# Optimization experiments

Hardware: AMD Instinct MI355X
Metric: run time of the kernel (lower is better)

The kernel has to match this reference:

```python
import jax, jax.numpy as jnp
import numpy as np

EMBED = 1024
HEADS = 16
HEAD_DIM = EMBED // HEADS


def setup_inputs() -> dict:
    key = jax.random.key(0)
    ks = jax.random.split(key, 8)
    N, L = 2, 2048
    s = 0.02
    return {
        "values": jax.random.normal(ks[0], (N, L, EMBED), jnp.float32),
        "keys": jax.random.normal(ks[1], (N, L, EMBED), jnp.float32),
        "queries": jax.random.normal(ks[2], (N, L, EMBED), jnp.float32),
        # per-head projection weights, SHARED across heads (nn.Linear(head_dim, head_dim))
        "Wv": jax.random.normal(ks[3], (HEAD_DIM, HEAD_DIM), jnp.float32) * s,
        "Wk": jax.random.normal(ks[4], (HEAD_DIM, HEAD_DIM), jnp.float32) * s,
        "Wq": jax.random.normal(ks[5], (HEAD_DIM, HEAD_DIM), jnp.float32) * s,
        "Wo": jax.random.normal(ks[6], (EMBED, EMBED), jnp.float32) * s,
        "bo": jax.random.normal(ks[7], (EMBED,), jnp.float32) * s,
    }


def reference(values, keys, queries, Wv, Wk, Wq, Wo, bo):
    N, Lq, _ = queries.shape
    Lk = keys.shape[1]
    Lv = values.shape[1]
    # split heads: (N, L, H, D)
    v = values.reshape(N, Lv, HEADS, HEAD_DIM)
    k = keys.reshape(N, Lk, HEADS, HEAD_DIM)
    q = queries.reshape(N, Lq, HEADS, HEAD_DIM)
    # per-head linear (weight shared across heads); nn.Linear computes x @ W.T
    v = jnp.einsum('nlhd,ed->nlhe', v, Wv)
    k = jnp.einsum('nlhd,ed->nlhe', k, Wk)
    q = jnp.einsum('nlhd,ed->nlhe', q, Wq)
    # scores (N, H, Lq, Lk); NOTE: scale uses sqrt(embed_size), as in the original
    scores = jnp.einsum('nqhd,nkhd->nhqk', q, k) / jnp.sqrt(jnp.float32(EMBED))
    attn = jax.nn.softmax(scores, axis=-1)
    out = jnp.einsum('nhql,nlhd->nqhd', attn, v).reshape(N, Lq, EMBED)
    out = out @ Wo.T + bo
    return out
```

## Files before the change

kernel.cpp:

```cpp
#include <hip/hip_runtime.h>
#include <hip/hip_bf16.h>

#define EMBED 1024
#define HEADS 16
#define HD 64
#define NB 2
#define LSEQ 2048

typedef __bf16 bf16x8 __attribute__((ext_vector_type(8)));
typedef float f32x4 __attribute__((ext_vector_type(4)));

static __device__ __forceinline__ __bf16 f2b(float x) {
    union { __hip_bfloat16 h; __bf16 b; } u;
    u.h = __float2bfloat16(x);
    return u.b;
}
static __device__ __forceinline__ bf16x8 cvt8(float4 a, float4 b) {
    bf16x8 r;
    r[0] = f2b(a.x); r[1] = f2b(a.y); r[2] = f2b(a.z); r[3] = f2b(a.w);
    r[4] = f2b(b.x); r[5] = f2b(b.y); r[6] = f2b(b.z); r[7] = f2b(b.w);
    return r;
}
static __device__ __forceinline__ unsigned short b2u(float x) {
    union { __hip_bfloat16 h; unsigned short u; } c;
    c.h = __float2bfloat16(x);
    return c.u;
}

#define GLD16(g, l) __builtin_amdgcn_global_load_lds( \
    (const __attribute__((address_space(1))) void*)(g), \
    (__attribute__((address_space(3))) void*)(l), 16, 0, 0)


__global__ __launch_bounds__(256) void proj_kernel(
    const float* __restrict__ vals,
    const float* __restrict__ keys,
    const float* __restrict__ quer,
    const float* __restrict__ Wv,
    const float* __restrict__ Wk,
    const float* __restrict__ Wq,
    __hip_bfloat16* __restrict__ QF,
    __hip_bfloat16* __restrict__ KF,
    __hip_bfloat16* __restrict__ VF)
{
    int b      = blockIdx.x;
    int tensor = b % 3;
    int rem    = b / 3;
    int n      = rem >> 7;
    int lt     = (rem >> 2) & 31;
    int hg     = rem & 3;
    int t = threadIdx.x, w = t >> 6, lane = t & 63;
    int m16 = lane & 15, quad = lane >> 4;
    int l0 = lt * 64 + w * 16;

    const float* X = (tensor == 0) ? quer : (tensor == 1 ? keys : vals);
    const float* W = (tensor == 0) ? Wq   : (tensor == 1 ? Wk   : Wv);
    float scale = (tensor == 0) ? (1.44269504088896340736f / 32.0f) : 1.0f;

    bf16x8 wf[4][2];
#pragma unroll
    for (int f = 0; f < 4; ++f)
#pragma unroll
        for (int kk = 0; kk < 2; ++kk) {
            const float* wp = W + (f * 16 + m16) * HD + kk * 32 + quad * 8;
            wf[f][kk] = cvt8(*(const float4*)wp, *(const float4*)(wp + 4));
        }

#pragma unroll
    for (int hh = 0; hh < 4; ++hh) {
        int h = hg * 4 + hh;
        const float* xb = X + ((size_t)n * LSEQ + l0 + m16) * EMBED + h * HD + quad * 8;
        bf16x8 xf[2];
#pragma unroll
        for (int kk = 0; kk < 2; ++kk)
            xf[kk] = cvt8(*(const float4*)(xb + kk * 32), *(const float4*)(xb + kk * 32 + 4));

        size_t nhb = (size_t)(n * HEADS + h) * 131072;
        if (tensor != 2) {
            f32x4 acc[4] = {};
#pragma unroll
            for (int f = 0; f < 4; ++f) {
                acc[f] = __builtin_amdgcn_mfma_f32_16x16x32_bf16(wf[f][0], xf[0], acc[f], 0, 0, 0);
                acc[f] = __builtin_amdgcn_mfma_f32_16x16x32_bf16(wf[f][1], xf[1], acc[f], 0, 0, 0);
            }
            int key = l0 + m16;
#pragma unroll
            for (int f = 0; f < 4; ++f) {
                union { ushort4 u; unsigned short s[4]; } p;
#pragma unroll
                for (int r = 0; r < 4; ++r) p.s[r] = b2u(acc[f][r] * scale);
                int kk   = f >> 1;
                int qk2  = (f & 1) * 2 + (quad >> 1);
                int j4   = (quad & 1) * 4;
                __hip_bfloat16* dst;
                if (tensor == 0) {
                    dst = QF + nhb + (size_t)(l0 >> 4) * 1024 + kk * 512
                        + (qk2 * 16 + m16) * 8 + j4;
                } else {
                    dst = KF + nhb + (size_t)(key >> 5) * 2048
                        + ((key & 1) * 2 + kk) * 512
                        + (qk2 * 16 + ((key & 31) >> 1)) * 8 + j4;
                }
                *(ushort4*)dst = p.u;
            }
        } else {
            f32x4 acc[4] = {};
#pragma unroll
            for (int f = 0; f < 4; ++f) {
                acc[f] = __builtin_amdgcn_mfma_f32_16x16x32_bf16(xf[0], wf[f][0], acc[f], 0, 0, 0);
                acc[f] = __builtin_amdgcn_mfma_f32_16x16x32_bf16(xf[1], wf[f][1], acc[f], 0, 0, 0);
            }
            int keyq  = l0 + quad * 4;
            int c     = keyq >> 5;
            int quadv = (keyq & 31) >> 3;
            int j4    = (quad & 1) * 4;
#pragma unroll
            for (int f = 0; f < 4; ++f) {
                union { ushort4 u; unsigned short s[4]; } p;
#pragma unroll
                for (int r = 0; r < 4; ++r) p.s[r] = b2u(acc[f][r]);
                __hip_bfloat16* dst = VF + nhb + (size_t)c * 2048 + f * 512
                    + quadv * 128 + m16 * 8 + j4;
                *(ushort4*)dst = p.u;
            }
        }
    }
}

__global__ __launch_bounds__(256) void wcvt_kernel(
    const float* __restrict__ Wo, __hip_bfloat16* __restrict__ Wob)
{
    int base = (blockIdx.x * 256 + threadIdx.x) * 16;
#pragma unroll
    for (int j = 0; j < 16; j += 4) {
        float4 w4 = *(const float4*)(Wo + base + j);
        __hip_bfloat16 o[4] = {
            __float2bfloat16(w4.x), __float2bfloat16(w4.y),
            __float2bfloat16(w4.z), __float2bfloat16(w4.w)};
        *(ushort4*)(Wob + base + j) = *(const ushort4*)o;
    }
}

#define CHUNKS 32
__global__ __launch_bounds__(256) void attn_kernel(
    const __hip_bfloat16* __restrict__ QF,
    const __hip_bfloat16* __restrict__ KF,
    const __hip_bfloat16* __restrict__ VF,
    __hip_bfloat16* __restrict__ AO)
{
    __shared__ __align__(16) __hip_bfloat16 Pb[2][4][32][40];

    int i  = blockIdx.x;
    int x  = i & 7, r2 = i >> 3;
    int nh = x * 4 + (r2 >> 5);
    int qblk = r2 & 31;

    int t = threadIdx.x, w = t >> 6, lane = t & 63;
    int m16 = lane & 15, quad = lane >> 4;
    int qh = w & 1, kh = w >> 1;
    int q0 = qblk * 64 + qh * 32;
    size_t nhb = (size_t)nh * 131072;

    const __hip_bfloat16* qb = QF + nhb + (size_t)(q0 >> 4) * 1024 + lane * 8;
    bf16x8 qf[2][2];
#pragma unroll
    for (int tq = 0; tq < 2; ++tq)
#pragma unroll
        for (int kk = 0; kk < 2; ++kk)
            qf[tq][kk] = *(const bf16x8*)(qb + tq * 1024 + kk * 512);

    const __hip_bfloat16* kp = KF + nhb + (size_t)(kh * 32) * 2048 + lane * 8;
    const __hip_bfloat16* vp = VF + nhb + (size_t)(kh * 32) * 2048 + lane * 8;

    f32x4 of[2][4] = {};
    float ls[2][4] = {};
    bf16x8 kf[2][2], vf[4], pf[2];

#pragma unroll 1
    for (int c = 0; c <= CHUNKS; ++c) {
        if (c < CHUNKS) {
            const __hip_bfloat16* kc = kp + (size_t)c * 2048;
            kf[0][0] = *(const bf16x8*)(kc);
            kf[0][1] = *(const bf16x8*)(kc + 512);
            kf[1][0] = *(const bf16x8*)(kc + 1024);
            kf[1][1] = *(const bf16x8*)(kc + 1536);
        }
        if (c > 0) {
            pf[0] = *(const bf16x8*)&Pb[(c - 1) & 1][w][m16][quad * 8];
            pf[1] = *(const bf16x8*)&Pb[(c - 1) & 1][w][16 + m16][quad * 8];
#pragma unroll
            for (int tq = 0; tq < 2; ++tq)
#pragma unroll
                for (int f = 0; f < 4; ++f)
                    of[tq][f] = __builtin_amdgcn_mfma_f32_16x16x32_bf16(
                        pf[tq], vf[f], of[tq][f], 0, 0, 0);
        }
        if (c < CHUNKS) {
            const __hip_bfloat16* vc = vp + (size_t)c * 2048;
#pragma unroll
            for (int f = 0; f < 4; ++f)
                vf[f] = *(const bf16x8*)(vc + f * 512);

            f32x4 s[2][2];
#pragma unroll
            for (int tq = 0; tq < 2; ++tq)
#pragma unroll
                for (int t2 = 0; t2 < 2; ++t2) {
                    f32x4 z = {};
                    z = __builtin_amdgcn_mfma_f32_16x16x32_bf16(qf[tq][0], kf[t2][0], z, 0, 0, 0);
                    z = __builtin_amdgcn_mfma_f32_16x16x32_bf16(qf[tq][1], kf[t2][1], z, 0, 0, 0);
                    s[tq][t2] = z;
                }
#pragma unroll
            for (int tq = 0; tq < 2; ++tq)
#pragma unroll
                for (int r = 0; r < 4; ++r) {
                    float e0 = __builtin_amdgcn_exp2f(s[tq][0][r]);
                    float e1 = __builtin_amdgcn_exp2f(s[tq][1][r]);
                    ls[tq][r] += e0 + e1;
                    unsigned u = __builtin_amdgcn_perm(
                        __float_as_uint(e1), __float_as_uint(e0), 0x07060302);
                    *(unsigned*)&Pb[c & 1][w][tq * 16 + quad * 4 + r][2 * m16] = u;
                }
        }
    }

#pragma unroll
    for (int tq = 0; tq < 2; ++tq)
#pragma unroll
        for (int r = 0; r < 4; ++r) {
            float v = ls[tq][r];
            v += __shfl_xor(v, 1);
            v += __shfl_xor(v, 2);
            v += __shfl_xor(v, 4);
            v += __shfl_xor(v, 8);
            ls[tq][r] = v;
        }

    __syncthreads();
    float* Cb = (float*)&Pb[0][0][0][0];
    if (kh == 1) {
        int base = qh * 2560;
#pragma unroll
        for (int tq = 0; tq < 2; ++tq)
#pragma unroll
            for (int f = 0; f < 4; ++f)
                *(f32x4*)&Cb[base + (tq * 4 + f) * 256 + lane * 4] = of[tq][f];
#pragma unroll
        for (int tq = 0; tq < 2; ++tq)
#pragma unroll
            for (int r = 0; r < 4; ++r)
                Cb[base + 2048 + (tq * 4 + r) * 64 + lane] = ls[tq][r];
    }
    __syncthreads();
    if (kh == 0) {
        int base = qh * 2560;
#pragma unroll
        for (int tq = 0; tq < 2; ++tq)
#pragma unroll
            for (int f = 0; f < 4; ++f)
                of[tq][f] += *(const f32x4*)&Cb[base + (tq * 4 + f) * 256 + lane * 4];
        int n = nh >> 4, h = nh & 15;
#pragma unroll
        for (int tq = 0; tq < 2; ++tq)
#pragma unroll
            for (int r = 0; r < 4; ++r) {
                float lt2 = ls[tq][r] + Cb[base + 2048 + (tq * 4 + r) * 64 + lane];
                float rinv = 1.0f / lt2;
                int qrow = q0 + tq * 16 + quad * 4 + r;
#pragma unroll
                for (int f = 0; f < 4; ++f) {
                    int col = h * HD + f * 16 + m16;
                    AO[((size_t)n * LSEQ + qrow) * EMBED + col] =
                        __float2bfloat16(of[tq][f][r] * rinv);
                }
            }
    }
}

__global__ __launch_bounds__(256) void outproj_kernel(
    const __hip_bfloat16* __restrict__ AO,
    const __hip_bfloat16* __restrict__ Wob,
    const float* __restrict__ bo,
    float* __restrict__ out)
{
    __shared__ __align__(16) __hip_bfloat16 As[128 * 32];
    __shared__ __align__(16) __hip_bfloat16 Bs[64 * 32];

    int b  = blockIdx.x;
    int mt = b >> 4, nt = b & 15;
    int m0 = mt * 128, n0 = nt * 64;
    int t = threadIdx.x, w = t >> 6, lane = t & 63;
    int m16 = lane & 15, quad = lane >> 4;

    int srow = lane >> 2;
    int scol = (lane & 3) * 8;

    const __hip_bfloat16* Ab = AO  + (size_t)m0 * EMBED;
    const __hip_bfloat16* Bb = Wob + (size_t)n0 * EMBED;

    f32x4 acc[2][4] = {};
    for (int k0 = 0; k0 < EMBED; k0 += 32) {
        __syncthreads();
#pragma unroll
        for (int j = 0; j < 2; ++j) {
            int g = j * 4 + w;
            GLD16(Ab + (size_t)(g * 16 + srow) * EMBED + k0 + scol, &As[g * 512]);
        }
        GLD16(Bb + (size_t)(w * 16 + srow) * EMBED + k0 + scol, &Bs[w * 512]);
        __syncthreads();

        bf16x8 af[2], bfr[4];
#pragma unroll
        for (int ta = 0; ta < 2; ++ta)
            af[ta] = *(const bf16x8*)&As[(w * 32 + ta * 16 + m16) * 32 + quad * 8];
#pragma unroll
        for (int tb = 0; tb < 4; ++tb)
            bfr[tb] = *(const bf16x8*)&Bs[(tb * 16 + m16) * 32 + quad * 8];
#pragma unroll
        for (int ta = 0; ta < 2; ++ta)
#pragma unroll
            for (int tb = 0; tb < 4; ++tb)
                acc[ta][tb] = __builtin_amdgcn_mfma_f32_16x16x32_bf16(
                    af[ta], bfr[tb], acc[ta][tb], 0, 0, 0);
    }

#pragma unroll
    for (int tb = 0; tb < 4; ++tb) {
        int col = n0 + tb * 16 + m16;
        float bias = bo[col];
#pragma unroll
        for (int ta = 0; ta < 2; ++ta)
#pragma unroll
            for (int r = 0; r < 4; ++r) {
                int row = m0 + w * 32 + ta * 16 + quad * 4 + r;
                out[(size_t)row * EMBED + col] = acc[ta][tb][r] + bias;
            }
    }
}

extern "C" void kernel_launch(void* const* d_in, const int* in_sizes, int n_in,
                              void* d_out, int out_size, void* d_ws, size_t ws_size,
                              hipStream_t stream) {
    const float* vals = (const float*)d_in[0];
    const float* keys = (const float*)d_in[1];
    const float* quer = (const float*)d_in[2];
    const float* Wv   = (const float*)d_in[3];
    const float* Wk   = (const float*)d_in[4];
    const float* Wq   = (const float*)d_in[5];
    const float* Wo   = (const float*)d_in[6];
    const float* bo   = (const float*)d_in[7];
    float* out = (float*)d_out;

    __hip_bfloat16* ws = (__hip_bfloat16*)d_ws;
    const size_t PE = (size_t)NB * HEADS * LSEQ * HD;
    __hip_bfloat16* QF  = ws;
    __hip_bfloat16* KF  = ws + PE;
    __hip_bfloat16* VF  = ws + 2 * PE;
    __hip_bfloat16* AO  = ws + 3 * PE;
    __hip_bfloat16* Wob = ws + 4 * PE;

    proj_kernel<<<3 * NB * (LSEQ / 64) * (HEADS / 4), 256, 0, stream>>>(
        vals, keys, quer, Wv, Wk, Wq, QF, KF, VF);
    wcvt_kernel<<<256, 256, 0, stream>>>(Wo, Wob);
    attn_kernel<<<1024, 256, 0, stream>>>(QF, KF, VF, AO);
    outproj_kernel<<<512, 256, 0, stream>>>(AO, Wob, bo, out);
}
```

Before: 186.0 us.

## Software-pipeline attention loop with double-buffered K and MFMA row sums

Restructures the attention main loop into a manually unrolled two-stage pipeline. K fragments are double-buffered so the next chunk's K loads are issued before the current score MFMAs. The softmax row-sum is now taken by an extra MFMA against a ones vector, which replaces the per-element float adds and the end-of-loop shuffle reduction; this sums the bf16-rounded probabilities. s_setprio wraps the MFMA bursts to favour matrix issue, at the cost of more registers and code size.

```diff
diff --git a/kernel.cpp b/kernel.cpp
--- a/kernel.cpp
+++ b/kernel.cpp
@@ -142,6 +142,64 @@
 }
 
 #define CHUNKS 32
+
+#define LOADK(KFR, c_) do { \
+    const __hip_bfloat16* kc_ = kp + (size_t)(c_) * 2048; \
+    KFR[0][0] = *(const bf16x8*)(kc_); \
+    KFR[0][1] = *(const bf16x8*)(kc_ + 512); \
+    KFR[1][0] = *(const bf16x8*)(kc_ + 1024); \
+    KFR[1][1] = *(const bf16x8*)(kc_ + 1536); \
+} while (0)
+
+#define LOADV(c_) do { \
+    const __hip_bfloat16* vc_ = vp + (size_t)(c_) * 2048; \
+    vf[0] = *(const bf16x8*)(vc_); \
+    vf[1] = *(const bf16x8*)(vc_ + 512); \
+    vf[2] = *(const bf16x8*)(vc_ + 1024); \
+    vf[3] = *(const bf16x8*)(vc_ + 1536); \
+} while (0)
+
+#define SCORE(KFR, BUF) do { \
+    f32x4 s_[2][2]; \
+    __builtin_amdgcn_s_setprio(1); \
+    _Pragma("unroll") \
+    for (int tq_ = 0; tq_ < 2; ++tq_) { \
+        _Pragma("unroll") \
+        for (int t2_ = 0; t2_ < 2; ++t2_) { \
+            f32x4 z_ = {}; \
+            z_ = __builtin_amdgcn_mfma_f32_16x16x32_bf16(qf[tq_][0], KFR[t2_][0], z_, 0, 0, 0); \
+            z_ = __builtin_amdgcn_mfma_f32_16x16x32_bf16(qf[tq_][1], KFR[t2_][1], z_, 0, 0, 0); \
+            s_[tq_][t2_] = z_; \
+        } \
+    } \
+    __builtin_amdgcn_s_setprio(0); \
+    _Pragma("unroll") \
+    for (int tq_ = 0; tq_ < 2; ++tq_) { \
+        _Pragma("unroll") \
+        for (int r_ = 0; r_ < 4; ++r_) { \
+            float e0_ = __builtin_amdgcn_exp2f(s_[tq_][0][r_]); \
+            float e1_ = __builtin_amdgcn_exp2f(s_[tq_][1][r_]); \
+            unsigned u_ = __builtin_amdgcn_perm( \
+                __float_as_uint(e1_), __float_as_uint(e0_), 0x07060302); \
+            *(unsigned*)&Pb[BUF][w][tq_ * 16 + quad * 4 + r_][2 * m16] = u_; \
+        } \
+    } \
+} while (0)
+
+#define PVSTEP(BUF) do { \
+    bf16x8 pf0_ = *(const bf16x8*)&Pb[BUF][w][m16][quad * 8]; \
+    bf16x8 pf1_ = *(const bf16x8*)&Pb[BUF][w][16 + m16][quad * 8]; \
+    __builtin_amdgcn_s_setprio(1); \
+    _Pragma("unroll") \
+    for (int f_ = 0; f_ < 4; ++f_) { \
+        of[0][f_] = __builtin_amdgcn_mfma_f32_16x16x32_bf16(pf0_, vf[f_], of[0][f_], 0, 0, 0); \
+        of[1][f_] = __builtin_amdgcn_mfma_f32_16x16x32_bf16(pf1_, vf[f_], of[1][f_], 0, 0, 0); \
+    } \
+    lsa[0] = __builtin_amdgcn_mfma_f32_16x16x32_bf16(pf0_, onesf, lsa[0], 0, 0, 0); \
+    lsa[1] = __builtin_amdgcn_mfma_f32_16x16x32_bf16(pf1_, onesf, lsa[1], 0, 0, 0); \
+    __builtin_amdgcn_s_setprio(0); \
+} while (0)
+
 __global__ __launch_bounds__(256) void attn_kernel(
     const __hip_bfloat16* __restrict__ QF,
     const __hip_bfloat16* __restrict__ KF,
@@ -172,70 +230,35 @@
     const __hip_bfloat16* kp = KF + nhb + (size_t)(kh * 32) * 2048 + lane * 8;
     const __hip_bfloat16* vp = VF + nhb + (size_t)(kh * 32) * 2048 + lane * 8;
 
+    bf16x8 onesf;
+#pragma unroll
+    for (int j = 0; j < 8; ++j) onesf[j] = f2b(1.0f);
+
     f32x4 of[2][4] = {};
-    float ls[2][4] = {};
-    bf16x8 kf[2][2], vf[4], pf[2];
+    f32x4 lsa[2] = {};
+    bf16x8 kfa[2][2], kfb[2][2], vf[4];
+
+    LOADK(kfa, 0);
+    LOADK(kfb, 1);
+    SCORE(kfa, 0);
+    LOADV(0);
 
 #pragma unroll 1
-    for (int c = 0; c <= CHUNKS; ++c) {
-        if (c < CHUNKS) {
-            const __hip_bfloat16* kc = kp + (size_t)c * 2048;
-            kf[0][0] = *(const bf16x8*)(kc);
-            kf[0][1] = *(const bf16x8*)(kc + 512);
-            kf[1][0] = *(const bf16x8*)(kc + 1024);
-            kf[1][1] = *(const bf16x8*)(kc + 1536);
-        }
-        if (c > 0) {
-            pf[0] = *(const bf16x8*)&Pb[(c - 1) & 1][w][m16][quad * 8];
-            pf[1] = *(const bf16x8*)&Pb[(c - 1) & 1][w][16 + m16][quad * 8];
-#pragma unroll
-            for (int tq = 0; tq < 2; ++tq)
-#pragma unroll
-                for (int f = 0; f < 4; ++f)
-                    of[tq][f] = __builtin_amdgcn_mfma_f32_16x16x32_bf16(
-                        pf[tq], vf[f], of[tq][f], 0, 0, 0);
-        }
-        if (c < CHUNKS) {
-            const __hip_bfloat16* vc = vp + (size_t)c * 2048;
-#pragma unroll
-            for (int f = 0; f < 4; ++f)
-                vf[f] = *(const bf16x8*)(vc + f * 512);
-
-            f32x4 s[2][2];
-#pragma unroll
-            for (int tq = 0; tq < 2; ++tq)
-#pragma unroll
-                for (int t2 = 0; t2 < 2; ++t2) {
-                    f32x4 z = {};
-                    z = __builtin_amdgcn_mfma_f32_16x16x32_bf16(qf[tq][0], kf[t2][0], z, 0, 0, 0);
-                    z = __builtin_amdgcn_mfma_f32_16x16x32_bf16(qf[tq][1], kf[t2][1], z, 0, 0, 0);
-                    s[tq][t2] = z;
-                }
-#pragma unroll
-            for (int tq = 0; tq < 2; ++tq)
-#pragma unroll
-                for (int r = 0; r < 4; ++r) {
-                    float e0 = __builtin_amdgcn_exp2f(s[tq][0][r]);
-                    float e1 = __builtin_amdgcn_exp2f(s[tq][1][r]);
-                    ls[tq][r] += e0 + e1;
-                    unsigned u = __builtin_amdgcn_perm(
-                        __float_as_uint(e1), __float_as_uint(e0), 0x07060302);
-                    *(unsigned*)&Pb[c & 1][w][tq * 16 + quad * 4 + r][2 * m16] = u;
-                }
-        }
-    }
-
-#pragma unroll
-    for (int tq = 0; tq < 2; ++tq)
-#pragma unroll
-        for (int r = 0; r < 4; ++r) {
-            float v = ls[tq][r];
-            v += __shfl_xor(v, 1);
-            v += __shfl_xor(v, 2);
-            v += __shfl_xor(v, 4);
-            v += __shfl_xor(v, 8);
-            ls[tq][r] = v;
-        }
+    for (int tt = 0; tt < 15; ++tt) {
+        int c = 2 * tt;
+        LOADK(kfa, c + 2);
+        SCORE(kfb, 1);
+        PVSTEP(0);
+        LOADV(c + 1);
+        LOADK(kfb, c + 3);
+        SCORE(kfa, 0);
+        PVSTEP(1);
+        LOADV(c + 2);
+    }
+    SCORE(kfb, 1);
+    PVSTEP(0);
+    LOADV(31);
+    PVSTEP(1);
 
     __syncthreads();
     float* Cb = (float*)&Pb[0][0][0][0];
@@ -250,7 +273,7 @@
         for (int tq = 0; tq < 2; ++tq)
 #pragma unroll
             for (int r = 0; r < 4; ++r)
-                Cb[base + 2048 + (tq * 4 + r) * 64 + lane] = ls[tq][r];
+                Cb[base + 2048 + (tq * 4 + r) * 64 + lane] = lsa[tq][r];
     }
     __syncthreads();
     if (kh == 0) {
@@ -265,7 +288,7 @@
         for (int tq = 0; tq < 2; ++tq)
 #pragma unroll
             for (int r = 0; r < 4; ++r) {
-                float lt2 = ls[tq][r] + Cb[base + 2048 + (tq * 4 + r) * 64 + lane];
+                float lt2 = lsa[tq][r] + Cb[base + 2048 + (tq * 4 + r) * 64 + lane];
                 float rinv = 1.0f / lt2;
                 int qrow = q0 + tq * 16 + quad * 4 + r;
 #pragma unroll
```

Result: faster. 176.2 us (-5.2%).
